# Kernel tuning notes

Hardware: AMD Instinct MI355X
Metric: run time of the kernel (lower is better)

Reference implementation:

```python
import jax, jax.numpy as jnp
import numpy as np

B, T, N, E = 64, 500, 21, 210
IN_DIM, HID, OUT_DIM = 1, 128, 1


def gcn_norm(edge_index, edge_weight, num_nodes):
    # PyG gcn_norm: add self loops (weight 1), deg over target nodes, symmetric normalization.
    src, dst = edge_index[0], edge_index[1]
    loop = jnp.arange(num_nodes)
    src = jnp.concatenate([src, loop])
    dst = jnp.concatenate([dst, loop])
    ew = jnp.concatenate([edge_weight, jnp.ones((num_nodes,), edge_weight.dtype)])
    deg = jnp.zeros((num_nodes,), edge_weight.dtype).at[dst].add(ew)
    dinv = jnp.where(deg > 0, deg ** -0.5, 0.0)
    norm = dinv[src] * ew * dinv[dst]
    # Dense N x N (N=21, tiny) normalized adjacency; out[i] = sum_j A[i, j] x[j].
    return jnp.zeros((num_nodes, num_nodes), edge_weight.dtype).at[dst, src].add(norm)


def _forward(edge_index, x, edge_weight, Wz_1, bz_1, lzw_1, lzb_1, Wr_1, br_1, lrw_1, lrb_1, Wh_1, bh_1, lhw_1, lhb_1, Wz_2, bz_2, lzw_2, lzb_2, Wr_2, br_2, lrw_2, lrb_2, Wh_2, bh_2, lhw_2, lhb_2, cls_w, cls_b):
    A = gcn_norm(edge_index, edge_weight, N)

    def gcn(X, W, b):  # X: (B, N, F)
        return jnp.einsum("ij,bjf->bif", A, X @ W) + b

    def cell(X, H, Wz, bz, lzw, lzb, Wr, br, lrw, lrb, Wh, bh, lhw, lhb):
        Z = jax.nn.sigmoid(jnp.concatenate([gcn(X, Wz, bz), H], -1) @ lzw + lzb)
        R = jax.nn.sigmoid(jnp.concatenate([gcn(X, Wr, br), H], -1) @ lrw + lrb)
        Ht = jnp.tanh(jnp.concatenate([gcn(X, Wh, bh), H * R], -1) @ lhw + lhb)
        return Z * H + (1.0 - Z) * Ht

    def step(carry, x_t):  # x_t: (B, N)
        H1, H2 = carry
        X = x_t[..., None]  # (B, N, 1)
        H1 = cell(X, H1, Wz_1, bz_1, lzw_1, lzb_1, Wr_1, br_1, lrw_1, lrb_1, Wh_1, bh_1, lhw_1, lhb_1)
        H2 = cell(H1, H2, Wz_2, bz_2, lzw_2, lzb_2, Wr_2, br_2, lrw_2, lrb_2, Wh_2, bh_2, lhw_2, lhb_2)
        return (H1, H2), H2.mean(axis=1)  # mean over nodes -> (B, HID)

    H0 = jnp.zeros((x.shape[0], N, HID), x.dtype)
    _, outs = jax.lax.scan(step, (H0, H0), jnp.moveaxis(x, 1, 0))  # outs: (T, B, HID)
    seq_out = outs.mean(axis=0)  # mean over time (== mean over nodes then time in original)
    return seq_out @ cls_w + cls_b  # (B, OUT_DIM)


def setup_inputs():
    key = jax.random.key(0)
    ks = list(jax.random.split(key, 20))
    kit = iter(ks)

    def nrm(shape, scale=0.05):
        return jax.random.normal(next(kit), shape, jnp.float32) * scale

    inp = {}
    inp["x"] = jax.random.normal(next(kit), (B, T, N), jnp.float32)
    inp["edge_index"] = jax.random.randint(next(kit), (2, E), 0, N)
    inp["edge_weight"] = jax.random.uniform(next(kit), (E,), jnp.float32)
    for tag, in_dim in (("1", IN_DIM), ("2", HID)):
        for g in "zrh":
            inp[f"W{g}_{tag}"] = nrm((in_dim, HID))
            inp[f"b{g}_{tag}"] = jnp.zeros((HID,), jnp.float32)
            inp[f"l{g}w_{tag}"] = nrm((2 * HID, HID))
            inp[f"l{g}b_{tag}"] = jnp.zeros((HID,), jnp.float32)
    inp["cls_w"] = nrm((HID, OUT_DIM))
    inp["cls_b"] = jnp.zeros((OUT_DIM,), jnp.float32)
    return inp


def reference(x, edge_index, edge_weight, Wz_1, bz_1, lzw_1, lzb_1, Wr_1, br_1, lrw_1, lrb_1, Wh_1, bh_1, lhw_1, lhb_1, Wz_2, bz_2, lzw_2, lzb_2, Wr_2, br_2, lrw_2, lrb_2, Wh_2, bh_2, lhw_2, lhb_2, cls_w, cls_b):
    return _forward(edge_index, x, edge_weight, Wz_1, bz_1, lzw_1, lzb_1, Wr_1, br_1, lrw_1, lrb_1, Wh_1, bh_1, lhw_1, lhb_1, Wz_2, bz_2, lzw_2, lzb_2, Wr_2, br_2, lrw_2, lrb_2, Wh_2, bh_2, lhw_2, lhb_2, cls_w, cls_b)
```

## Files before the change

kernel.cpp:

```cpp
#include <hip/hip_runtime.h>
#include <hip/hip_bf16.h>


#define NN 21
#define NROW 24
#define HID 128
#define TSTEPS 500
#define EDGES 210
#define NTHREADS 512
#define RPT 6

#define WS_A     0
#define WS_VEC   1600
#define WS_LZR1  3200
#define WS_LH1   36000
#define WS_WE2   52400
#define WS_LZR2  101600
#define WS_LH2   134400

#define WAVE_SYNC() asm volatile("s_waitcnt lgkmcnt(0)" ::: "memory")

typedef float v2f __attribute__((ext_vector_type(2)));

__device__ __forceinline__ v2f lo2(float4 w) { v2f v = {w.x, w.y}; return v; }
__device__ __forceinline__ v2f hi2(float4 w) { v2f v = {w.z, w.w}; return v; }
__device__ __forceinline__ void pkf(v2f& acc, float s, v2f w) {
    v2f ss = {s, s};
    acc = __builtin_elementwise_fma(ss, w, acc);
}
__device__ __forceinline__ float sigmoidf(float v) {
    return 1.0f / (1.0f + expf(-v));
}

__global__ void build_A(const int* __restrict__ ei, const float* __restrict__ ew,
                        float* __restrict__ Aout) {
    __shared__ double deg[NN];
    __shared__ double dinv[NN];
    __shared__ double Asm[NN * NN];
    int t = threadIdx.x;
    for (int k = t; k < NN * NN; k += blockDim.x) Asm[k] = 0.0;
    if (t < NN) deg[t] = 1.0;
    __syncthreads();
    if (t == 0) {
        for (int e = 0; e < EDGES; e++) deg[ei[EDGES + e]] += (double)ew[e];
        for (int i = 0; i < NN; i++) dinv[i] = deg[i] > 0.0 ? 1.0 / sqrt(deg[i]) : 0.0;
        for (int e = 0; e < EDGES; e++) {
            int s = ei[e], d = ei[EDGES + e];
            Asm[d * NN + s] += dinv[s] * (double)ew[e] * dinv[d];
        }
        for (int i = 0; i < NN; i++) Asm[i * NN + i] += dinv[i] * dinv[i];
    }
    __syncthreads();
    for (int k = t; k < NROW * NN; k += blockDim.x)
        Aout[k] = (k < NN * NN) ? (float)Asm[k] : 0.0f;
}

__global__ void pack_bot(const float* __restrict__ w0, const float* __restrict__ w1,
                         float4* __restrict__ out, int ngate) {
    int t = blockIdx.x * blockDim.x + threadIdx.x;
    int per_c = ngate * 128;
    int total = 32 * per_c;
    if (t >= total) return;
    int c = t / per_c, rem = t - c * per_c;
    int gate = rem >> 7;
    int r2 = rem & 127;
    int k2 = r2 >> 6;
    int f0 = r2 & 63;
    int k = 4 * c + 2 * k2;
    const float* src = (gate == 0) ? w0 : w1;
    float4 v;
    v.x = src[(128 + k) * 128 + f0];
    v.y = src[(128 + k) * 128 + f0 + 64];
    v.z = src[(128 + k + 1) * 128 + f0];
    v.w = src[(128 + k + 1) * 128 + f0 + 64];
    out[t] = v;
}

__global__ void make_weff2(const float* __restrict__ Wz2, const float* __restrict__ Wr2,
                           const float* __restrict__ Wh2,
                           const float* __restrict__ lzw2, const float* __restrict__ lrw2,
                           const float* __restrict__ lhw2,
                           float4* __restrict__ out) {
    int t = blockIdx.x * blockDim.x + threadIdx.x;
    if (t >= 32 * 384) return;
    int c = t / 384, rem = t - c * 384;
    int g = rem >> 7;
    int r2 = rem & 127;
    int k2 = r2 >> 6;
    int f0 = r2 & 63;
    int k = 4 * c + 2 * k2;
    const float* W = (g == 0) ? Wz2 : (g == 1) ? Wr2 : Wh2;
    const float* L = (g == 0) ? lzw2 : (g == 1) ? lrw2 : lhw2;
    double a0 = 0, a1 = 0, a2 = 0, a3 = 0;
    for (int m = 0; m < 128; m++) {
        double w0 = (double)W[k * 128 + m];
        double w1 = (double)W[(k + 1) * 128 + m];
        a0 += w0 * (double)L[m * 128 + f0];
        a1 += w0 * (double)L[m * 128 + f0 + 64];
        a2 += w1 * (double)L[m * 128 + f0];
        a3 += w1 * (double)L[m * 128 + f0 + 64];
    }
    out[t] = make_float4((float)a0, (float)a1, (float)a2, (float)a3);
}

__global__ void make_vecs(const float* __restrict__ Wz1, const float* __restrict__ Wr1,
                          const float* __restrict__ Wh1,
                          const float* __restrict__ bz1, const float* __restrict__ br1,
                          const float* __restrict__ bh1,
                          const float* __restrict__ lzw1, const float* __restrict__ lrw1,
                          const float* __restrict__ lhw1,
                          const float* __restrict__ lzb1, const float* __restrict__ lrb1,
                          const float* __restrict__ lhb1,
                          const float* __restrict__ bz2, const float* __restrict__ br2,
                          const float* __restrict__ bh2,
                          const float* __restrict__ lzw2, const float* __restrict__ lrw2,
                          const float* __restrict__ lhw2,
                          const float* __restrict__ lzb2, const float* __restrict__ lrb2,
                          const float* __restrict__ lhb2,
                          float* __restrict__ out) {
    int t = blockIdx.x * blockDim.x + threadIdx.x;
    if (t >= 9 * 128) return;
    int v = t >> 7, f = t & 127;
    double acc = 0.0;
    if (v < 3) {
        const float* W = (v == 0) ? Wz1 : (v == 1) ? Wr1 : Wh1;
        const float* L = (v == 0) ? lzw1 : (v == 1) ? lrw1 : lhw1;
        for (int m = 0; m < 128; m++) acc += (double)W[m] * (double)L[m * 128 + f];
    } else if (v < 6) {
        int g = v - 3;
        const float* bb = (g == 0) ? bz1 : (g == 1) ? br1 : bh1;
        const float* L  = (g == 0) ? lzw1 : (g == 1) ? lrw1 : lhw1;
        const float* lb = (g == 0) ? lzb1 : (g == 1) ? lrb1 : lhb1;
        for (int m = 0; m < 128; m++) acc += (double)bb[m] * (double)L[m * 128 + f];
        acc += (double)lb[f];
    } else {
        int g = v - 6;
        const float* bb = (g == 0) ? bz2 : (g == 1) ? br2 : bh2;
        const float* L  = (g == 0) ? lzw2 : (g == 1) ? lrw2 : lhw2;
        const float* lb = (g == 0) ? lzb2 : (g == 1) ? lrb2 : lhb2;
        for (int m = 0; m < 128; m++) acc += (double)bb[m] * (double)L[m * 128 + f];
        acc += (double)lb[f];
    }
    out[t] = (float)acc;
}

__global__ __launch_bounds__(NTHREADS, 1) void tgcn_main(
    const float* __restrict__ x,
    const float* __restrict__ ws,
    const float* __restrict__ cls_w,
    const float* __restrict__ cls_b,
    float* __restrict__ out)
{
    const int b  = blockIdx.x;
    const int t  = threadIdx.x;
    const bool isA = (t < 256);
    const int lt = t & 255;
    const int f0 = lt & 63;
    const int f1 = f0 + 64;
    const int gw = __builtin_amdgcn_readfirstlane(lt >> 6);
    const int iA = gw * RPT;
    const int nreal = (iA + RPT <= NN) ? RPT : (NN - iA);

    __shared__ __align__(16) float sH1[2][NROW * HID];
    __shared__ __align__(16) float sH2[NROW * HID];
    __shared__ __align__(16) float sHR1[NROW * HID];
    __shared__ __align__(16) float sHR2[NROW * HID];
    __shared__ __align__(16) float sAH[NROW * HID];
    __shared__ float sA[NROW * NN];
    __shared__ float sax[2][NROW];
    __shared__ double sred[4][HID];

    const float*  vecs = ws + WS_VEC;
    const float4* Lzr1 = (const float4*)(ws + WS_LZR1);
    const float4* Lh1  = (const float4*)(ws + WS_LH1);
    const float4* We2  = (const float4*)(ws + WS_WE2);
    const float4* Lzr2 = (const float4*)(ws + WS_LZR2);
    const float4* Lh2  = (const float4*)(ws + WS_LH2);

    const float4* H2v  = (const float4*)sH2;
    const float4* HR1v = (const float4*)sHR1;
    const float4* HR2v = (const float4*)sHR2;
    const float4* AHv  = (const float4*)sAH;

    for (int k = t; k < 2 * NROW * HID; k += NTHREADS) ((float*)sH1)[k] = 0.0f;
    for (int k = t; k < NROW * HID; k += NTHREADS) sH2[k] = 0.0f;
    for (int k = t; k < NROW * NN; k += NTHREADS) sA[k] = ws[WS_A + k];

    const v2f wz1v = {vecs[f0],        vecs[f1]};
    const v2f wr1v = {vecs[128 + f0],  vecs[128 + f1]};
    const v2f wh1v = {vecs[256 + f0],  vecs[256 + f1]};
    const v2f cz1v = {vecs[384 + f0],  vecs[384 + f1]};
    const v2f cr1v = {vecs[512 + f0],  vecs[512 + f1]};
    const v2f ch1v = {vecs[640 + f0],  vecs[640 + f1]};
    const v2f cz2v = {vecs[768 + f0],  vecs[768 + f1]};
    const v2f cr2v = {vecs[896 + f0],  vecs[896 + f1]};
    const v2f ch2v = {vecs[1024 + f0], vecs[1024 + f1]};

    __syncthreads();

    const float* xb = x + (size_t)b * (TSTEPS * NN);
    if (t < NROW) {
        float a0s = 0.0f, a1s = 0.0f;
        for (int j = 0; j < NN; j++) {
            a0s = fmaf(sA[t * NN + j], xb[j], a0s);
            a1s = fmaf(sA[t * NN + j], xb[NN + j], a1s);
        }
        sax[0][t] = a0s;
        sax[1][t] = a1s;
    }
    __syncthreads();

    double oacc0 = 0.0, oacc1 = 0.0;

    auto layer1 = [&](int s) {
        const float* H1rd = sH1[(s + 1) & 1];
        float*       H1wr = sH1[s & 1];
        const float4* H1c = (const float4*)H1rd;
        float axp[RPT];
        #pragma unroll
        for (int r = 0; r < RPT; r++) axp[r] = sax[s & 1][iA + r];
        v2f az[RPT], ar[RPT];
        #pragma unroll
        for (int r = 0; r < RPT; r++) {
            az[r] = __builtin_elementwise_fma((v2f){axp[r], axp[r]}, wz1v, cz1v);
            ar[r] = __builtin_elementwise_fma((v2f){axp[r], axp[r]}, wr1v, cr1v);
        }
        #pragma unroll 2
        for (int c = 0; c < 32; ++c) {
            const float4 wz0 = Lzr1[c * 256 + f0];
            const float4 wz1 = Lzr1[c * 256 + 64 + f0];
            const float4 wr0 = Lzr1[c * 256 + 128 + f0];
            const float4 wr1 = Lzr1[c * 256 + 192 + f0];
            #pragma unroll
            for (int r = 0; r < RPT; r++) {
                const float4 h = H1c[(iA + r) * 32 + c];
                pkf(az[r], h.x, lo2(wz0)); pkf(az[r], h.y, hi2(wz0));
                pkf(az[r], h.z, lo2(wz1)); pkf(az[r], h.w, hi2(wz1));
                pkf(ar[r], h.x, lo2(wr0)); pkf(ar[r], h.y, hi2(wr0));
                pkf(ar[r], h.z, lo2(wr1)); pkf(ar[r], h.w, hi2(wr1));
            }
        }
        v2f zg[RPT], h1c[RPT];
        #pragma unroll
        for (int r = 0; r < RPT; r++) {
            zg[r].x = sigmoidf(az[r].x);
            zg[r].y = sigmoidf(az[r].y);
            const float r0 = sigmoidf(ar[r].x);
            const float r1 = sigmoidf(ar[r].y);
            h1c[r].x = H1rd[(iA + r) * HID + f0];
            h1c[r].y = H1rd[(iA + r) * HID + f1];
            sHR1[(iA + r) * HID + f0] = h1c[r].x * r0;
            sHR1[(iA + r) * HID + f1] = h1c[r].y * r1;
        }
        WAVE_SYNC();
        v2f ah[RPT];
        #pragma unroll
        for (int r = 0; r < RPT; r++)
            ah[r] = __builtin_elementwise_fma((v2f){axp[r], axp[r]}, wh1v, ch1v);
        #pragma unroll 2
        for (int c = 0; c < 32; ++c) {
            const float4 wh0 = Lh1[c * 128 + f0];
            const float4 wh1 = Lh1[c * 128 + 64 + f0];
            #pragma unroll
            for (int r = 0; r < RPT; r++) {
                const float4 q = HR1v[(iA + r) * 32 + c];
                pkf(ah[r], q.x, lo2(wh0)); pkf(ah[r], q.y, hi2(wh0));
                pkf(ah[r], q.z, lo2(wh1)); pkf(ah[r], q.w, hi2(wh1));
            }
        }
        #pragma unroll
        for (int r = 0; r < RPT; r++) {
            const float n0 = fmaf(zg[r].x, h1c[r].x, (1.0f - zg[r].x) * tanhf(ah[r].x));
            const float n1 = fmaf(zg[r].y, h1c[r].y, (1.0f - zg[r].y) * tanhf(ah[r].y));
            H1wr[(iA + r) * HID + f0] = n0;
            H1wr[(iA + r) * HID + f1] = n1;
        }
    };

    if (isA) layer1(0);
    __syncthreads();

    for (int k = 0; k < TSTEPS; k++) {
        if (isA) {
            if (k + 1 < TSTEPS) {
                layer1(k + 1);
                if (t < NROW && k + 2 < TSTEPS) {
                    const float* xt = xb + (size_t)(k + 2) * NN;
                    float a = 0.0f;
                    for (int j = 0; j < NN; j++) a = fmaf(sA[t * NN + j], xt[j], a);
                    sax[(k + 2) & 1][t] = a;
                }
            }
        } else {
            const float* H1rd = sH1[k & 1];
            v2f aa[RPT];
            #pragma unroll
            for (int r = 0; r < RPT; r++) aa[r] = (v2f){0.0f, 0.0f};
            #pragma unroll 3
            for (int j = 0; j < NN; j++) {
                const v2f hj = {H1rd[j * HID + f0], H1rd[j * HID + f1]};
                #pragma unroll
                for (int r = 0; r < RPT; r++) {
                    const float arj = sA[(iA + r) * NN + j];
                    aa[r] = __builtin_elementwise_fma((v2f){arj, arj}, hj, aa[r]);
                }
            }
            #pragma unroll
            for (int r = 0; r < RPT; r++) {
                sAH[(iA + r) * HID + f0] = aa[r].x;
                sAH[(iA + r) * HID + f1] = aa[r].y;
            }
            WAVE_SYNC();
            v2f pz[RPT], pr[RPT], ph[RPT];
            #pragma unroll
            for (int r = 0; r < RPT; r++) { pz[r] = cz2v; pr[r] = cr2v; ph[r] = ch2v; }
            for (int c = 0; c < 32; ++c) {
                const float4 wz0 = We2[c * 384 + f0];
                const float4 wz1 = We2[c * 384 + 64 + f0];
                const float4 wr0 = We2[c * 384 + 128 + f0];
                const float4 wr1 = We2[c * 384 + 192 + f0];
                const float4 wh0 = We2[c * 384 + 256 + f0];
                const float4 wh1 = We2[c * 384 + 320 + f0];
                const float4 lz0 = Lzr2[c * 256 + f0];
                const float4 lz1 = Lzr2[c * 256 + 64 + f0];
                const float4 lr0 = Lzr2[c * 256 + 128 + f0];
                const float4 lr1 = Lzr2[c * 256 + 192 + f0];
                #pragma unroll
                for (int r = 0; r < RPT; r++) {
                    const float4 a = AHv[(iA + r) * 32 + c];
                    const float4 q = H2v[(iA + r) * 32 + c];
                    pkf(pz[r], a.x, lo2(wz0)); pkf(pz[r], a.y, hi2(wz0));
                    pkf(pz[r], a.z, lo2(wz1)); pkf(pz[r], a.w, hi2(wz1));
                    pkf(pz[r], q.x, lo2(lz0)); pkf(pz[r], q.y, hi2(lz0));
                    pkf(pz[r], q.z, lo2(lz1)); pkf(pz[r], q.w, hi2(lz1));
                    pkf(pr[r], a.x, lo2(wr0)); pkf(pr[r], a.y, hi2(wr0));
                    pkf(pr[r], a.z, lo2(wr1)); pkf(pr[r], a.w, hi2(wr1));
                    pkf(pr[r], q.x, lo2(lr0)); pkf(pr[r], q.y, hi2(lr0));
                    pkf(pr[r], q.z, lo2(lr1)); pkf(pr[r], q.w, hi2(lr1));
                    pkf(ph[r], a.x, lo2(wh0)); pkf(ph[r], a.y, hi2(wh0));
                    pkf(ph[r], a.z, lo2(wh1)); pkf(ph[r], a.w, hi2(wh1));
                }
            }
            v2f z2[RPT], h2c[RPT];
            #pragma unroll
            for (int r = 0; r < RPT; r++) {
                z2[r].x = sigmoidf(pz[r].x);
                z2[r].y = sigmoidf(pz[r].y);
                const float r20 = sigmoidf(pr[r].x);
                const float r21 = sigmoidf(pr[r].y);
                h2c[r].x = sH2[(iA + r) * HID + f0];
                h2c[r].y = sH2[(iA + r) * HID + f1];
                sHR2[(iA + r) * HID + f0] = h2c[r].x * r20;
                sHR2[(iA + r) * HID + f1] = h2c[r].y * r21;
            }
            WAVE_SYNC();
            #pragma unroll 2
            for (int c = 0; c < 32; ++c) {
                const float4 lh0 = Lh2[c * 128 + f0];
                const float4 lh1 = Lh2[c * 128 + 64 + f0];
                #pragma unroll
                for (int r = 0; r < RPT; r++) {
                    const float4 q = HR2v[(iA + r) * 32 + c];
                    pkf(ph[r], q.x, lo2(lh0)); pkf(ph[r], q.y, hi2(lh0));
                    pkf(ph[r], q.z, lo2(lh1)); pkf(ph[r], q.w, hi2(lh1));
                }
            }
            #pragma unroll
            for (int r = 0; r < RPT; r++) {
                const float m0 = fmaf(z2[r].x, h2c[r].x, (1.0f - z2[r].x) * tanhf(ph[r].x));
                const float m1 = fmaf(z2[r].y, h2c[r].y, (1.0f - z2[r].y) * tanhf(ph[r].y));
                sH2[(iA + r) * HID + f0] = m0;
                sH2[(iA + r) * HID + f1] = m1;
                if (r < nreal) {
                    oacc0 += (double)m0;
                    oacc1 += (double)m1;
                }
            }
        }
        __syncthreads();
    }

    if (!isA) {
        sred[gw][f0] = oacc0;
        sred[gw][f1] = oacc1;
    }
    __syncthreads();
    if (t < HID) {
        double s = 0.0;
        for (int gg = 0; gg < 4; gg++) s += sred[gg][t];
        sred[0][t] = (s / (double)(TSTEPS * NN)) * (double)cls_w[t];
    }
    __syncthreads();
    if (t < 64) {
        double v = ((double*)sred)[t] + ((double*)sred)[t + 64];
        for (int off = 32; off; off >>= 1) v += __shfl_down(v, off, 64);
        if (t == 0) out[b] = (float)(v + (double)cls_b[0]);
    }
}

extern "C" void kernel_launch(void* const* d_in, const int* in_sizes, int n_in,
                              void* d_out, int out_size, void* d_ws, size_t ws_size,
                              hipStream_t stream) {
    const float* x    = (const float*)d_in[0];
    const int*   ei   = (const int*)  d_in[1];
    const float* ew   = (const float*)d_in[2];
    const float* Wz1  = (const float*)d_in[3];
    const float* bz1  = (const float*)d_in[4];
    const float* lzw1 = (const float*)d_in[5];
    const float* lzb1 = (const float*)d_in[6];
    const float* Wr1  = (const float*)d_in[7];
    const float* br1  = (const float*)d_in[8];
    const float* lrw1 = (const float*)d_in[9];
    const float* lrb1 = (const float*)d_in[10];
    const float* Wh1  = (const float*)d_in[11];
    const float* bh1  = (const float*)d_in[12];
    const float* lhw1 = (const float*)d_in[13];
    const float* lhb1 = (const float*)d_in[14];
    const float* Wz2  = (const float*)d_in[15];
    const float* bz2  = (const float*)d_in[16];
    const float* lzw2 = (const float*)d_in[17];
    const float* lzb2 = (const float*)d_in[18];
    const float* Wr2  = (const float*)d_in[19];
    const float* br2  = (const float*)d_in[20];
    const float* lrw2 = (const float*)d_in[21];
    const float* lrb2 = (const float*)d_in[22];
    const float* Wh2  = (const float*)d_in[23];
    const float* bh2  = (const float*)d_in[24];
    const float* lhw2 = (const float*)d_in[25];
    const float* lhb2 = (const float*)d_in[26];
    const float* clsw = (const float*)d_in[27];
    const float* clsb = (const float*)d_in[28];

    float* ws   = (float*)d_ws;
    float* outp = (float*)d_out;

    build_A<<<1, 64, 0, stream>>>(ei, ew, ws + WS_A);
    pack_bot<<<32, 256, 0, stream>>>(lzw1, lrw1, (float4*)(ws + WS_LZR1), 2);
    pack_bot<<<16, 256, 0, stream>>>(lhw1, lhw1, (float4*)(ws + WS_LH1), 1);
    pack_bot<<<32, 256, 0, stream>>>(lzw2, lrw2, (float4*)(ws + WS_LZR2), 2);
    pack_bot<<<16, 256, 0, stream>>>(lhw2, lhw2, (float4*)(ws + WS_LH2), 1);
    make_weff2<<<48, 256, 0, stream>>>(Wz2, Wr2, Wh2, lzw2, lrw2, lhw2,
                                       (float4*)(ws + WS_WE2));
    make_vecs<<<5, 256, 0, stream>>>(Wz1, Wr1, Wh1, bz1, br1, bh1,
                                     lzw1, lrw1, lhw1, lzb1, lrb1, lhb1,
                                     bz2, br2, bh2, lzw2, lrw2, lhw2,
                                     lzb2, lrb2, lhb2, ws + WS_VEC);
    tgcn_main<<<64, NTHREADS, 0, stream>>>(x, ws, clsw, clsb, outp);
}
```

Baseline: 12.53 ms.

## Split layer-1 and layer-2 GRU cells into separate producer/consumer blocks

Replaces the single 512-thread block per batch with two 256-thread blocks per batch. One block computes the layer-1 cell and streams each new H1 through a double-buffered global ring. The other block computes the layer-2 cell, and the two stay in step through agent-scope flag spinning. This lets the layers pipeline across time steps on separate CUs instead of running serially within one block. The cost is cross-CU synchronization latency, cache-bypassing global traffic per step, and a deadlock risk if not all 128 blocks are co-resident. The new path runs only when the workspace is large enough; otherwise the old kernel is used.

```diff
diff --git a/kernel.cpp b/kernel.cpp
--- a/kernel.cpp
+++ b/kernel.cpp
@@ -7,7 +7,6 @@
 #define HID 128
 #define TSTEPS 500
 #define EDGES 210
-#define NTHREADS 512
 #define RPT 6
 
 #define WS_A     0
@@ -17,8 +16,13 @@
 #define WS_WE2   52400
 #define WS_LZR2  101600
 #define WS_LH2   134400
+#define WS_FLAGS 150784
+#define WS_RING  154880
+#define RING_SLOT 3072
+#define WS_END   (WS_RING + 64 * 2 * RING_SLOT)
 
 #define WAVE_SYNC() asm volatile("s_waitcnt lgkmcnt(0)" ::: "memory")
+#define VM_SYNC()   asm volatile("s_waitcnt vmcnt(0)" ::: "memory")
 
 typedef float v2f __attribute__((ext_vector_type(2)));
 
@@ -30,6 +34,9 @@
 }
 __device__ __forceinline__ float sigmoidf(float v) {
     return 1.0f / (1.0f + expf(-v));
+}
+__device__ __forceinline__ void dc_store(float* p, float v) {
+    asm volatile("global_store_dword %0, %1, off sc0 sc1" :: "v"(p), "v"(v) : "memory");
 }
 
 __global__ void build_A(const int* __restrict__ ei, const float* __restrict__ ew,
@@ -53,6 +60,11 @@
     __syncthreads();
     for (int k = t; k < NROW * NN; k += blockDim.x)
         Aout[k] = (k < NN * NN) ? (float)Asm[k] : 0.0f;
+}
+
+__global__ void init_flags(unsigned* f) {
+    int i = blockIdx.x * blockDim.x + threadIdx.x;
+    if (i < 4096) f[i] = 0u;
 }
 
 __global__ void pack_bot(const float* __restrict__ w0, const float* __restrict__ w1,
@@ -144,11 +156,314 @@
     out[t] = (float)acc;
 }
 
+__global__ __launch_bounds__(256, 1) void tgcn_split(
+    const float* __restrict__ x, float* __restrict__ ws,
+    const float* __restrict__ cls_w, const float* __restrict__ cls_b,
+    float* __restrict__ out)
+{
+    const int bid = blockIdx.x;
+    const bool roleA = (bid < 64);
+    const int b  = bid & 63;
+    const int t  = threadIdx.x;
+    const int f0 = t & 63;
+    const int f1 = f0 + 64;
+    const int gw = __builtin_amdgcn_readfirstlane(t >> 6);
+    const int iA = gw * RPT;
+    const int nreal = (iA + RPT <= NN) ? RPT : (NN - iA);
+
+    unsigned* fwdp  = (unsigned*)(ws + WS_FLAGS) + b * 32;
+    unsigned* backp = (unsigned*)(ws + WS_FLAGS) + 2048 + b * 32;
+    float* ringB = ws + WS_RING + (size_t)b * (2 * RING_SLOT);
+
+    __shared__ __align__(16) float sH1[2][NROW * HID];
+    __shared__ __align__(16) float sHR1[NROW * HID];
+    __shared__ __align__(16) float sH1B[NROW * HID];
+    __shared__ __align__(16) float sH2[NROW * HID];
+    __shared__ __align__(16) float sHR2[NROW * HID];
+    __shared__ __align__(16) float sAH[NROW * HID];
+    __shared__ float sA[NROW * NN];
+    __shared__ float sax[2][NROW];
+    __shared__ double sred[4][HID];
+
+    const float*  vecs = ws + WS_VEC;
+    const float4* Lzr1 = (const float4*)(ws + WS_LZR1);
+    const float4* Lh1  = (const float4*)(ws + WS_LH1);
+    const float4* We2  = (const float4*)(ws + WS_WE2);
+    const float4* Lzr2 = (const float4*)(ws + WS_LZR2);
+    const float4* Lh2  = (const float4*)(ws + WS_LH2);
+
+    const float4* HR1v = (const float4*)sHR1;
+    const float4* HR2v = (const float4*)sHR2;
+    const float4* AHv  = (const float4*)sAH;
+    const float4* H2v  = (const float4*)sH2;
+
+    for (int k = t; k < 2 * NROW * HID; k += 256) ((float*)sH1)[k] = 0.0f;
+    for (int k = t; k < NROW * HID; k += 256) {
+        sH2[k] = 0.0f; sHR1[k] = 0.0f; sHR2[k] = 0.0f; sAH[k] = 0.0f; sH1B[k] = 0.0f;
+    }
+    for (int k = t; k < NROW * NN; k += 256) sA[k] = ws[WS_A + k];
+
+    const v2f wz1v = {vecs[f0],        vecs[f1]};
+    const v2f wr1v = {vecs[128 + f0],  vecs[128 + f1]};
+    const v2f wh1v = {vecs[256 + f0],  vecs[256 + f1]};
+    const v2f cz1v = {vecs[384 + f0],  vecs[384 + f1]};
+    const v2f cr1v = {vecs[512 + f0],  vecs[512 + f1]};
+    const v2f ch1v = {vecs[640 + f0],  vecs[640 + f1]};
+    const v2f cz2v = {vecs[768 + f0],  vecs[768 + f1]};
+    const v2f cr2v = {vecs[896 + f0],  vecs[896 + f1]};
+    const v2f ch2v = {vecs[1024 + f0], vecs[1024 + f1]};
+
+    __syncthreads();
+
+    if (roleA) {
+        const float* xb = x + (size_t)b * (TSTEPS * NN);
+        if (t < NROW) {
+            float a0s = 0.0f, a1s = 0.0f;
+            for (int j = 0; j < NN; j++) {
+                a0s = fmaf(sA[t * NN + j], xb[j], a0s);
+                a1s = fmaf(sA[t * NN + j], xb[NN + j], a1s);
+            }
+            sax[0][t] = a0s;
+            sax[1][t] = a1s;
+        }
+        __syncthreads();
+
+        for (int s = 0; s < TSTEPS; s++) {
+            if (t == 0 && s >= 2) {
+                while (__hip_atomic_load(backp, __ATOMIC_RELAXED,
+                                         __HIP_MEMORY_SCOPE_AGENT) < (unsigned)(s - 1))
+                    __builtin_amdgcn_s_sleep(2);
+            }
+            __syncthreads();
+
+            {
+                const float* H1rd = sH1[(s + 1) & 1];
+                float*       H1wr = sH1[s & 1];
+                const float4* H1c = (const float4*)H1rd;
+                float* g = ringB + (s & 1) * RING_SLOT;
+                float axp[RPT];
+                #pragma unroll
+                for (int r = 0; r < RPT; r++) axp[r] = sax[s & 1][iA + r];
+                v2f az[RPT], ar[RPT];
+                #pragma unroll
+                for (int r = 0; r < RPT; r++) {
+                    az[r] = __builtin_elementwise_fma((v2f){axp[r], axp[r]}, wz1v, cz1v);
+                    ar[r] = __builtin_elementwise_fma((v2f){axp[r], axp[r]}, wr1v, cr1v);
+                }
+                #pragma unroll 2
+                for (int c = 0; c < 32; ++c) {
+                    const float4 wz0 = Lzr1[c * 256 + f0];
+                    const float4 wz1 = Lzr1[c * 256 + 64 + f0];
+                    const float4 wr0 = Lzr1[c * 256 + 128 + f0];
+                    const float4 wr1 = Lzr1[c * 256 + 192 + f0];
+                    #pragma unroll
+                    for (int r = 0; r < RPT; r++) {
+                        const float4 h = H1c[(iA + r) * 32 + c];
+                        pkf(az[r], h.x, lo2(wz0)); pkf(az[r], h.y, hi2(wz0));
+                        pkf(az[r], h.z, lo2(wz1)); pkf(az[r], h.w, hi2(wz1));
+                        pkf(ar[r], h.x, lo2(wr0)); pkf(ar[r], h.y, hi2(wr0));
+                        pkf(ar[r], h.z, lo2(wr1)); pkf(ar[r], h.w, hi2(wr1));
+                    }
+                }
+                v2f zg[RPT], h1c[RPT];
+                #pragma unroll
+                for (int r = 0; r < RPT; r++) {
+                    zg[r].x = sigmoidf(az[r].x);
+                    zg[r].y = sigmoidf(az[r].y);
+                    const float r0 = sigmoidf(ar[r].x);
+                    const float r1 = sigmoidf(ar[r].y);
+                    h1c[r].x = H1rd[(iA + r) * HID + f0];
+                    h1c[r].y = H1rd[(iA + r) * HID + f1];
+                    sHR1[(iA + r) * HID + f0] = h1c[r].x * r0;
+                    sHR1[(iA + r) * HID + f1] = h1c[r].y * r1;
+                }
+                WAVE_SYNC();
+                v2f ah[RPT];
+                #pragma unroll
+                for (int r = 0; r < RPT; r++)
+                    ah[r] = __builtin_elementwise_fma((v2f){axp[r], axp[r]}, wh1v, ch1v);
+                #pragma unroll 2
+                for (int c = 0; c < 32; ++c) {
+                    const float4 wh0 = Lh1[c * 128 + f0];
+                    const float4 wh1 = Lh1[c * 128 + 64 + f0];
+                    #pragma unroll
+                    for (int r = 0; r < RPT; r++) {
+                        const float4 q = HR1v[(iA + r) * 32 + c];
+                        pkf(ah[r], q.x, lo2(wh0)); pkf(ah[r], q.y, hi2(wh0));
+                        pkf(ah[r], q.z, lo2(wh1)); pkf(ah[r], q.w, hi2(wh1));
+                    }
+                }
+                #pragma unroll
+                for (int r = 0; r < RPT; r++) {
+                    const int row = iA + r;
+                    const float n0 = fmaf(zg[r].x, h1c[r].x, (1.0f - zg[r].x) * tanhf(ah[r].x));
+                    const float n1 = fmaf(zg[r].y, h1c[r].y, (1.0f - zg[r].y) * tanhf(ah[r].y));
+                    H1wr[row * HID + f0] = n0;
+                    H1wr[row * HID + f1] = n1;
+                    dc_store(g + row * HID + f0, n0);
+                    dc_store(g + row * HID + f1, n1);
+                }
+            }
+            if (t < NROW && s + 2 < TSTEPS) {
+                const float* xt = xb + (size_t)(s + 2) * NN;
+                float a = 0.0f;
+                for (int j = 0; j < NN; j++) a = fmaf(sA[t * NN + j], xt[j], a);
+                sax[(s + 2) & 1][t] = a;
+            }
+            VM_SYNC();
+            __syncthreads();
+            if (t == 0)
+                __hip_atomic_store(fwdp, (unsigned)(s + 1), __ATOMIC_RELAXED,
+                                   __HIP_MEMORY_SCOPE_AGENT);
+        }
+        return;
+    }
+
+    double oacc0 = 0.0, oacc1 = 0.0;
+    v2f ph[RPT], z2[RPT], h2c[RPT];
+
+    auto l2_p5 = [&]() {
+        #pragma unroll 2
+        for (int c = 0; c < 32; ++c) {
+            const float4 lh0 = Lh2[c * 128 + f0];
+            const float4 lh1 = Lh2[c * 128 + 64 + f0];
+            #pragma unroll
+            for (int r = 0; r < RPT; r++) {
+                const float4 q = HR2v[(iA + r) * 32 + c];
+                pkf(ph[r], q.x, lo2(lh0)); pkf(ph[r], q.y, hi2(lh0));
+                pkf(ph[r], q.z, lo2(lh1)); pkf(ph[r], q.w, hi2(lh1));
+            }
+        }
+        #pragma unroll
+        for (int r = 0; r < RPT; r++) {
+            const float m0 = fmaf(z2[r].x, h2c[r].x, (1.0f - z2[r].x) * tanhf(ph[r].x));
+            const float m1 = fmaf(z2[r].y, h2c[r].y, (1.0f - z2[r].y) * tanhf(ph[r].y));
+            sH2[(iA + r) * HID + f0] = m0;
+            sH2[(iA + r) * HID + f1] = m1;
+            if (r < nreal) {
+                oacc0 += (double)m0;
+                oacc1 += (double)m1;
+            }
+        }
+    };
+
+    for (int k = 0; k < TSTEPS; k++) {
+        if (k >= 1) l2_p5();
+        if (t == 0) {
+            while (__hip_atomic_load(fwdp, __ATOMIC_RELAXED,
+                                     __HIP_MEMORY_SCOPE_AGENT) < (unsigned)(k + 1))
+                __builtin_amdgcn_s_sleep(2);
+        }
+        __syncthreads();
+        {
+            const float4* gs = (const float4*)(ringB + (k & 1) * RING_SLOT);
+            const float4* p0 = gs + t;
+            const float4* p1 = gs + t + 256;
+            const float4* p2 = gs + t + 512;
+            float4 v0, v1, v2;
+            asm volatile(
+                "global_load_dwordx4 %0, %3, off sc0 sc1\n\t"
+                "global_load_dwordx4 %1, %4, off sc0 sc1\n\t"
+                "global_load_dwordx4 %2, %5, off sc0 sc1\n\t"
+                "s_waitcnt vmcnt(0)"
+                : "=v"(v0), "=v"(v1), "=v"(v2)
+                : "v"(p0), "v"(p1), "v"(p2)
+                : "memory");
+            float4* sB = (float4*)sH1B;
+            sB[t] = v0; sB[t + 256] = v1; sB[t + 512] = v2;
+        }
+        WAVE_SYNC();
+        __syncthreads();
+        if (t == 0)
+            __hip_atomic_store(backp, (unsigned)(k + 1), __ATOMIC_RELAXED,
+                               __HIP_MEMORY_SCOPE_AGENT);
+        {
+            v2f aa[RPT];
+            #pragma unroll
+            for (int r = 0; r < RPT; r++) aa[r] = (v2f){0.0f, 0.0f};
+            #pragma unroll 3
+            for (int j = 0; j < NN; j++) {
+                const v2f hj = {sH1B[j * HID + f0], sH1B[j * HID + f1]};
+                #pragma unroll
+                for (int r = 0; r < RPT; r++) {
+                    const float arj = sA[(iA + r) * NN + j];
+                    aa[r] = __builtin_elementwise_fma((v2f){arj, arj}, hj, aa[r]);
+                }
+            }
+            #pragma unroll
+            for (int r = 0; r < RPT; r++) {
+                sAH[(iA + r) * HID + f0] = aa[r].x;
+                sAH[(iA + r) * HID + f1] = aa[r].y;
+            }
+        }
+        WAVE_SYNC();
+        {
+            v2f pz[RPT], pr[RPT];
+            #pragma unroll
+            for (int r = 0; r < RPT; r++) { pz[r] = cz2v; pr[r] = cr2v; ph[r] = ch2v; }
+            for (int c = 0; c < 32; ++c) {
+                const float4 wz0 = We2[c * 384 + f0];
+                const float4 wz1 = We2[c * 384 + 64 + f0];
+                const float4 wr0 = We2[c * 384 + 128 + f0];
+                const float4 wr1 = We2[c * 384 + 192 + f0];
+                const float4 wh0 = We2[c * 384 + 256 + f0];
+                const float4 wh1 = We2[c * 384 + 320 + f0];
+                const float4 lz0 = Lzr2[c * 256 + f0];
+                const float4 lz1 = Lzr2[c * 256 + 64 + f0];
+                const float4 lr0 = Lzr2[c * 256 + 128 + f0];
+                const float4 lr1 = Lzr2[c * 256 + 192 + f0];
+                #pragma unroll
+                for (int r = 0; r < RPT; r++) {
+                    const float4 a = AHv[(iA + r) * 32 + c];
+                    const float4 q = H2v[(iA + r) * 32 + c];
+                    pkf(pz[r], a.x, lo2(wz0)); pkf(pz[r], a.y, hi2(wz0));
+                    pkf(pz[r], a.z, lo2(wz1)); pkf(pz[r], a.w, hi2(wz1));
+                    pkf(pz[r], q.x, lo2(lz0)); pkf(pz[r], q.y, hi2(lz0));
+                    pkf(pz[r], q.z, lo2(lz1)); pkf(pz[r], q.w, hi2(lz1));
+                    pkf(pr[r], a.x, lo2(wr0)); pkf(pr[r], a.y, hi2(wr0));
+                    pkf(pr[r], a.z, lo2(wr1)); pkf(pr[r], a.w, hi2(wr1));
+                    pkf(pr[r], q.x, lo2(lr0)); pkf(pr[r], q.y, hi2(lr0));
+                    pkf(pr[r], q.z, lo2(lr1)); pkf(pr[r], q.w, hi2(lr1));
+                    pkf(ph[r], a.x, lo2(wh0)); pkf(ph[r], a.y, hi2(wh0));
+                    pkf(ph[r], a.z, lo2(wh1)); pkf(ph[r], a.w, hi2(wh1));
+                }
+            }
+            #pragma unroll
+            for (int r = 0; r < RPT; r++) {
+                z2[r].x = sigmoidf(pz[r].x);
+                z2[r].y = sigmoidf(pz[r].y);
+                const float r20 = sigmoidf(pr[r].x);
+                const float r21 = sigmoidf(pr[r].y);
+                h2c[r].x = sH2[(iA + r) * HID + f0];
+                h2c[r].y = sH2[(iA + r) * HID + f1];
+                sHR2[(iA + r) * HID + f0] = h2c[r].x * r20;
+                sHR2[(iA + r) * HID + f1] = h2c[r].y * r21;
+            }
+        }
+        WAVE_SYNC();
+    }
+
+    l2_p5();
+    sred[gw][f0] = oacc0;
+    sred[gw][f1] = oacc1;
+    __syncthreads();
+    if (t < HID) {
+        double s = 0.0;
+        for (int gg = 0; gg < 4; gg++) s += sred[gg][t];
+        sred[0][t] = (s / (double)(TSTEPS * NN)) * (double)cls_w[t];
+    }
+    __syncthreads();
+    if (t < 64) {
+        double v = ((double*)sred)[t] + ((double*)sred)[t + 64];
+        for (int off = 32; off; off >>= 1) v += __shfl_down(v, off, 64);
+        if (t == 0) out[b] = (float)(v + (double)cls_b[0]);
+    }
+}
+
+#define NTHREADS 512
 __global__ __launch_bounds__(NTHREADS, 1) void tgcn_main(
-    const float* __restrict__ x,
-    const float* __restrict__ ws,
-    const float* __restrict__ cls_w,
-    const float* __restrict__ cls_b,
+    const float* __restrict__ x, const float* __restrict__ ws,
+    const float* __restrict__ cls_w, const float* __restrict__ cls_b,
     float* __restrict__ out)
 {
     const int b  = blockIdx.x;
@@ -445,5 +760,12 @@
                                      lzw1, lrw1, lhw1, lzb1, lrb1, lhb1,
                                      bz2, br2, bh2, lzw2, lrw2, lhw2,
                                      lzb2, lrb2, lhb2, ws + WS_VEC);
-    tgcn_main<<<64, NTHREADS, 0, stream>>>(x, ws, clsw, clsb, outp);
-}
+
+    const size_t need = (size_t)WS_END * sizeof(float);
+    if (ws_size >= need) {
+        init_flags<<<16, 256, 0, stream>>>((unsigned*)(ws + WS_FLAGS));
+        tgcn_split<<<128, 256, 0, stream>>>(x, ws, clsw, clsb, outp);
+    } else {
+        tgcn_main<<<64, NTHREADS, 0, stream>>>(x, ws, clsw, clsb, outp);
+    }
+}
```

After: 10.08 ms. 1.24x faster.
